# Performance work log

Hardware: AMD Instinct MI355X
Metric: run time of the kernel (lower is better)

The kernel has to match this reference:

```python
import jax, jax.numpy as jnp
import numpy as np

EPS = 1e-06
N_HEADS = 8


def setup_inputs() -> dict:
    key = jax.random.key(0)
    ks = jax.random.split(key, 9)
    B, M, T, C = 2, 64, 256, 512
    s = 0.02
    return {
        "x": jax.random.normal(ks[0], (B, M, T, C), dtype=jnp.float32),
        "Wq": jax.random.normal(ks[1], (C, C), dtype=jnp.float32) * s,
        "bq": jnp.zeros((C,), dtype=jnp.float32),
        "Wk": jax.random.normal(ks[2], (C, C), dtype=jnp.float32) * s,
        "bk": jnp.zeros((C,), dtype=jnp.float32),
        "Wv": jax.random.normal(ks[3], (C, C), dtype=jnp.float32) * s,
        "bv": jnp.zeros((C,), dtype=jnp.float32),
        "Wp": jax.random.normal(ks[4], (C, C), dtype=jnp.float32) * s,
        "bp": jnp.zeros((C,), dtype=jnp.float32),
    }


def _proj_heads(x, W, b, N, D):
    # nn.Linear: x @ W.T + b, then view(B,M,T,N,D).transpose(2,3) -> [B,M,N,T,D]
    B, M, T, C = x.shape
    y = jnp.einsum('bmtc,dc->bmtd', x, W) + b
    return y.reshape(B, M, T, N, D).transpose(0, 1, 3, 2, 4)


def reference(x, Wq, bq, Wk, bk, Wv, bv, Wp, bp):
    B, M, T, C = x.shape
    N = N_HEADS
    D = C // N
    q = _proj_heads(x, Wq, bq, N, D)  # [B,M,N,T,D]
    k = _proj_heads(x, Wk, bk, N, D)
    v = _proj_heads(x, Wv, bv, N, D)
    # ELU+1 feature map
    q = jax.nn.elu(q) + 1.0
    k = jax.nn.elu(k) + 1.0
    # KtV = k^T @ v : [B,M,N,D,D]
    KtV = jnp.einsum('bmntd,bmnte->bmnde', k, v)
    # Z = 1 / (q @ sum_t k + eps) : [B,M,N,T]
    ksum = jnp.sum(k, axis=-2)  # [B,M,N,D]
    z = 1.0 / (jnp.einsum('bmntd,bmnd->bmnt', q, ksum) + EPS)
    # Original does Z.expand(...,D) @ KtV; since Z is constant over the D axis,
    # this equals z[t] * sum_d KtV[d, e] -- compute that directly (faithful math).
    KtV_colsum = jnp.sum(KtV, axis=-2)  # [B,M,N,D]
    V = z[..., None] * KtV_colsum[..., None, :]  # [B,M,N,T,D]
    V = V.transpose(0, 1, 3, 2, 4).reshape(B, M, T, N * D)
    out = jnp.einsum('bmtc,dc->bmtd', V, Wp) + bp
    return out
```

## Files before the change

### kernel.cpp

```cpp
#include <hip/hip_runtime.h>
#include <hip/hip_bf16.h>

#define BM_ 128
#define T_  256
#define C_  512
#define NH  8
#define DH  64

typedef __bf16 bf16;
typedef __attribute__((ext_vector_type(8))) __bf16 bf16x8;
typedef __attribute__((ext_vector_type(4))) float f32x4;

__device__ __forceinline__ float elu1(float v){ return v > 0.f ? v + 1.f : __expf(v); }

__device__ __forceinline__ unsigned short f2bf(float f){
  unsigned u = __float_as_uint(f);
  u += 0x7fffu + ((u >> 16) & 1u);
  return (unsigned short)(u >> 16);
}

__device__ __forceinline__ float bf2f(unsigned short b){
  return __uint_as_float(((unsigned)b) << 16);
}

#define GLOAD16(gptr, lptr) __builtin_amdgcn_global_load_lds( \
  (const __attribute__((address_space(1))) void*)(gptr), \
  (__attribute__((address_space(3))) void*)(lptr), 16, 0, 0)

#define FENCE() asm volatile("" ::: "memory")

__global__ __launch_bounds__(256) void cvt3_kernel(
    const float* __restrict__ a, int na4,
    const float* __restrict__ b, int nb4,
    const float* __restrict__ c, int nc4,
    unsigned short* __restrict__ oa, unsigned short* __restrict__ ob,
    unsigned short* __restrict__ oc)
{
  int i = blockIdx.x * blockDim.x + threadIdx.x;
  int stride = gridDim.x * blockDim.x;
  int total = na4 + nb4 + nc4;
  for (; i < total; i += stride) {
    const float* src; unsigned short* dst; int idx;
    if (i < na4)            { src = a; dst = oa; idx = i; }
    else if (i < na4 + nb4) { src = b; dst = ob; idx = i - na4; }
    else                    { src = c; dst = oc; idx = i - na4 - nb4; }
    float4 v = reinterpret_cast<const float4*>(src)[idx];
    ushort4 o;
    o.x = f2bf(v.x); o.y = f2bf(v.y); o.z = f2bf(v.z); o.w = f2bf(v.w);
    reinterpret_cast<ushort4*>(dst)[idx] = o;
  }
}

template<int MODE>
__global__ __launch_bounds__(512, 2) void gemm_proj(
    const bf16* __restrict__ A, const bf16* __restrict__ Bw,
    const float* __restrict__ bias,
    float* __restrict__ krow, float* __restrict__ ksum2,
    const float* __restrict__ ksum2_in, float* __restrict__ zden)
{
  __shared__ bf16 As[2][256 * 64];
  __shared__ bf16 Bs[2][256 * 64];

  const int tid  = threadIdx.x;
  const int lane = tid & 63;
  const int wid  = tid >> 6;
  const int wr   = wid >> 2, wc = wid & 3;

  const int L  = ((blockIdx.x & 7) << 5) + (blockIdx.x >> 3);
  const int tn = L & 1, tm = L >> 1;

  const bf16* Ab = A  + (size_t)(tm * 256) * C_;
  const bf16* Bb = Bw + (size_t)(tn * 256) * C_;

  const int srow  = tid >> 3;
  const int sslot = tid & 7;
  const int fr = lane & 15, fq = lane >> 4;

  f32x4 acc[8][4];
#pragma unroll
  for (int m = 0; m < 8; ++m)
#pragma unroll
    for (int n = 0; n < 4; ++n) acc[m][n] = (f32x4){0.f, 0.f, 0.f, 0.f};

#define STG(XS, Xb, b, h, kt) do { \
  _Pragma("unroll") \
  for (int q = 0; q < 2; ++q) { \
    int r_ = (h) * 128 + q * 64 + srow; \
    GLOAD16(Xb + (size_t)r_ * C_ + (kt) * 64 + ((sslot ^ (r_ & 7)) << 3), \
            &XS[b][(((h) * 128 + q * 64) << 6) + (tid << 3)]); \
  } } while (0)

#define LOFF(row, sl) (((row) << 6) + ((((sl) ^ ((row) & 7))) << 3))

  STG(As, Ab, 0, 0, 0); STG(As, Ab, 0, 1, 0);
  STG(Bs, Bb, 0, 0, 0); STG(Bs, Bb, 0, 1, 0);
  asm volatile("s_waitcnt vmcnt(0)" ::: "memory");
  __builtin_amdgcn_s_barrier();
  FENCE();

  bf16x8 af[4][2], bfr[4][2];

  for (int t = 0; t < 8; ++t) {
    const int cur = t & 1;
    const bool pre = (t < 7);
#pragma unroll
    for (int m = 0; m < 4; ++m)
#pragma unroll
      for (int kk = 0; kk < 2; ++kk) {
        int row = wr * 128 + m * 16 + fr;
        af[m][kk] = *reinterpret_cast<const bf16x8*>(&As[cur][LOFF(row, kk * 4 + fq)]);
      }
#pragma unroll
    for (int n = 0; n < 2; ++n)
#pragma unroll
      for (int kk = 0; kk < 2; ++kk) {
        int row = wc * 64 + n * 16 + fr;
        bfr[n][kk] = *reinterpret_cast<const bf16x8*>(&Bs[cur][LOFF(row, kk * 4 + fq)]);
      }
    if (pre) { STG(As, Ab, cur ^ 1, 0, t + 1); STG(Bs, Bb, cur ^ 1, 0, t + 1); }
    __builtin_amdgcn_s_setprio(1);
#pragma unroll
    for (int m = 0; m < 4; ++m)
#pragma unroll
      for (int n = 0; n < 2; ++n)
#pragma unroll
        for (int kk = 0; kk < 2; ++kk)
          acc[m][n] = __builtin_amdgcn_mfma_f32_16x16x32_bf16(af[m][kk], bfr[n][kk], acc[m][n], 0, 0, 0);
    __builtin_amdgcn_s_setprio(0);
    __builtin_amdgcn_s_barrier();
    FENCE();
#pragma unroll
    for (int n = 0; n < 2; ++n)
#pragma unroll
      for (int kk = 0; kk < 2; ++kk) {
        int row = wc * 64 + (n + 2) * 16 + fr;
        bfr[n + 2][kk] = *reinterpret_cast<const bf16x8*>(&Bs[cur][LOFF(row, kk * 4 + fq)]);
      }
    if (pre) STG(As, Ab, cur ^ 1, 1, t + 1);
    __builtin_amdgcn_s_setprio(1);
#pragma unroll
    for (int m = 0; m < 4; ++m)
#pragma unroll
      for (int n = 0; n < 2; ++n)
#pragma unroll
        for (int kk = 0; kk < 2; ++kk)
          acc[m][n + 2] = __builtin_amdgcn_mfma_f32_16x16x32_bf16(af[m][kk], bfr[n + 2][kk], acc[m][n + 2], 0, 0, 0);
    __builtin_amdgcn_s_setprio(0);
    __builtin_amdgcn_s_barrier();
    FENCE();
#pragma unroll
    for (int m = 0; m < 4; ++m)
#pragma unroll
      for (int kk = 0; kk < 2; ++kk) {
        int row = wr * 128 + 64 + m * 16 + fr;
        af[m][kk] = *reinterpret_cast<const bf16x8*>(&As[cur][LOFF(row, kk * 4 + fq)]);
      }
    if (pre) STG(Bs, Bb, cur ^ 1, 1, t + 1);
    __builtin_amdgcn_s_setprio(1);
#pragma unroll
    for (int m = 0; m < 4; ++m)
#pragma unroll
      for (int n = 0; n < 2; ++n)
#pragma unroll
        for (int kk = 0; kk < 2; ++kk)
          acc[m + 4][n] = __builtin_amdgcn_mfma_f32_16x16x32_bf16(af[m][kk], bfr[n][kk], acc[m + 4][n], 0, 0, 0);
    __builtin_amdgcn_s_setprio(0);
    __builtin_amdgcn_s_barrier();
    FENCE();
    __builtin_amdgcn_s_setprio(1);
#pragma unroll
    for (int m = 0; m < 4; ++m)
#pragma unroll
      for (int n = 0; n < 2; ++n)
#pragma unroll
        for (int kk = 0; kk < 2; ++kk)
          acc[m + 4][n + 2] = __builtin_amdgcn_mfma_f32_16x16x32_bf16(af[m][kk], bfr[n + 2][kk], acc[m + 4][n + 2], 0, 0, 0);
    __builtin_amdgcn_s_setprio(0);
    asm volatile("s_waitcnt vmcnt(0)" ::: "memory");
    __builtin_amdgcn_s_barrier();
    FENCE();
  }
#undef STG
#undef LOFF

  const int bm   = tm;
  const int head = tn * 4 + wc;
  float bj[4];
#pragma unroll
  for (int n = 0; n < 4; ++n) bj[n] = bias[tn * 256 + wc * 64 + n * 16 + fr];

  if (MODE == 0) {
    float cs[4] = {0.f, 0.f, 0.f, 0.f};
#pragma unroll
    for (int m = 0; m < 8; ++m) {
#pragma unroll
      for (int r = 0; r < 4; ++r) {
        float rs = 0.f;
#pragma unroll
        for (int n = 0; n < 4; ++n) {
          float v = elu1(acc[m][n][r] + bj[n]);
          rs += v;
          cs[n] += v;
        }
#pragma unroll
        for (int msk = 1; msk < 16; msk <<= 1) rs += __shfl_xor(rs, msk);
        if (fr == 0) {
          int tg = wr * 128 + m * 16 + fq * 4 + r;
          krow[((size_t)bm * NH + head) * T_ + tg] = rs;
        }
      }
    }
#pragma unroll
    for (int n = 0; n < 4; ++n) {
      cs[n] += __shfl_xor(cs[n], 16);
      cs[n] += __shfl_xor(cs[n], 32);
      if (fq == 0)
        ksum2[((size_t)wr * BM_ + bm) * C_ + tn * 256 + wc * 64 + n * 16 + fr] = cs[n];
    }
  } else {
    float ks[4];
#pragma unroll
    for (int n = 0; n < 4; ++n) {
      size_t col = (size_t)bm * C_ + tn * 256 + wc * 64 + n * 16 + fr;
      ks[n] = ksum2_in[col] + ksum2_in[(size_t)BM_ * C_ + col];
    }
#pragma unroll
    for (int m = 0; m < 8; ++m) {
#pragma unroll
      for (int r = 0; r < 4; ++r) {
        float zs = 0.f;
#pragma unroll
        for (int n = 0; n < 4; ++n) zs = fmaf(elu1(acc[m][n][r] + bj[n]), ks[n], zs);
#pragma unroll
        for (int msk = 1; msk < 16; msk <<= 1) zs += __shfl_xor(zs, msk);
        if (fr == 0) {
          int tg = wr * 128 + m * 16 + fq * 4 + r;
          zden[((size_t)bm * NH + head) * T_ + tg] = zs;
        }
      }
    }
  }
}

__global__ __launch_bounds__(256) void xk_kernel(
    const unsigned short* __restrict__ xb, const float* __restrict__ krow,
    float* __restrict__ xk4, float* __restrict__ srow4)
{
  const int bm = blockIdx.x, qt = blockIdx.y, tid = threadIdx.x;
  __shared__ float krs[NH * 64];
#pragma unroll
  for (int p = 0; p < 2; ++p) {
    int idx = tid + p * 256;
    int n = idx >> 6, t = idx & 63;
    krs[idx] = krow[((size_t)bm * NH + n) * T_ + qt * 64 + t];
  }
  __syncthreads();
  float a0[8], a1[8];
#pragma unroll
  for (int n = 0; n < 8; ++n) { a0[n] = 0.f; a1[n] = 0.f; }
  const unsigned short* xp = xb + ((size_t)bm * T_ + qt * 64) * C_ + tid * 2;
  for (int t = 0; t < 64; ++t) {
    ushort2 u = *reinterpret_cast<const ushort2*>(xp + (size_t)t * C_);
    float x0 = bf2f(u.x), x1 = bf2f(u.y);
#pragma unroll
    for (int n = 0; n < 8; ++n) {
      float kr = krs[n * 64 + t];
      a0[n] = fmaf(kr, x0, a0[n]);
      a1[n] = fmaf(kr, x1, a1[n]);
    }
  }
#pragma unroll
  for (int n = 0; n < 8; ++n)
    *reinterpret_cast<float2*>(&xk4[(((size_t)qt * BM_ + bm) * NH + n) * C_ + tid * 2])
        = make_float2(a0[n], a1[n]);
  if (tid < 8) {
    float s = 0.f;
    for (int t = 0; t < 64; ++t) s += krs[tid * 64 + t];
    srow4[((size_t)qt * BM_ + bm) * NH + tid] = s;
  }
}

__global__ __launch_bounds__(256) void colsum_kernel(
    const float* __restrict__ xk4, const float* __restrict__ srow4,
    const float* __restrict__ Wv, const float* __restrict__ bv,
    float* __restrict__ cs_g)
{
  const int bm0 = blockIdx.x * 8, h = blockIdx.y, tid = threadIdx.x;
  __shared__ float4 xs4[8][128];
#pragma unroll
  for (int p = 0; p < 4; ++p) {
    int idx = tid + p * 256;
    int bmr = idx >> 7, c4 = idx & 127;
    float4 s = make_float4(0.f, 0.f, 0.f, 0.f);
#pragma unroll
    for (int q = 0; q < 4; ++q) {
      float4 u = *reinterpret_cast<const float4*>(
          xk4 + (((size_t)q * BM_ + bm0 + bmr) * NH + h) * C_ + c4 * 4);
      s.x += u.x; s.y += u.y; s.z += u.z; s.w += u.w;
    }
    xs4[bmr][c4] = s;
  }
  __syncthreads();
  const int e = tid & 63, bs = tid >> 6;
  const float4* wv4 = reinterpret_cast<const float4*>(Wv + (size_t)(h * DH + e) * C_);
  float acc0 = 0.f, acc1 = 0.f;
#pragma unroll 4
  for (int c4 = 0; c4 < 128; ++c4) {
    float4 w = wv4[c4];
    float4 a = xs4[bs * 2][c4];
    float4 b = xs4[bs * 2 + 1][c4];
    acc0 += w.x * a.x + w.y * a.y + w.z * a.z + w.w * a.w;
    acc1 += w.x * b.x + w.y * b.y + w.z * b.z + w.w * b.w;
  }
  float bve = bv[h * DH + e];
  int bmA = bm0 + bs * 2, bmB = bmA + 1;
  float sA = 0.f, sB = 0.f;
#pragma unroll
  for (int q = 0; q < 4; ++q) {
    sA += srow4[((size_t)q * BM_ + bmA) * NH + h];
    sB += srow4[((size_t)q * BM_ + bmB) * NH + h];
  }
  cs_g[((size_t)bmA * NH + h) * DH + e] = acc0 + sA * bve;
  cs_g[((size_t)bmB * NH + h) * DH + e] = acc1 + sB * bve;
}

__global__ __launch_bounds__(256) void wbuf_kernel(
    const float* __restrict__ cs_g, const float* __restrict__ Wp,
    float* __restrict__ wbuf)
{
  const int cpt = blockIdx.x, h = blockIdx.y, bm0 = blockIdx.z * 16;
  const int tid = threadIdx.x;
  __shared__ float4 csL4[16][16];
  {
    int bmr = tid >> 4, e4 = tid & 15;
    csL4[bmr][e4] = *reinterpret_cast<const float4*>(
        cs_g + ((size_t)(bm0 + bmr) * NH + h) * DH + e4 * 4);
  }
  __syncthreads();
  const int cp = cpt * 256 + tid;
  float4 wp[16];
  const float4* wpr = reinterpret_cast<const float4*>(Wp + (size_t)cp * C_ + h * DH);
#pragma unroll
  for (int e4 = 0; e4 < 16; ++e4) wp[e4] = wpr[e4];
#pragma unroll
  for (int bmr = 0; bmr < 16; ++bmr) {
    float acc = 0.f;
#pragma unroll
    for (int e4 = 0; e4 < 16; ++e4) {
      float4 c = csL4[bmr][e4];
      acc += wp[e4].x * c.x + wp[e4].y * c.y + wp[e4].z * c.z + wp[e4].w * c.w;
    }
    wbuf[((size_t)(bm0 + bmr) * NH + h) * C_ + cp] = acc;
  }
}

__global__ __launch_bounds__(256) void out_kernel(
    const float* __restrict__ zden, const float* __restrict__ wbuf,
    const float* __restrict__ bp, float* __restrict__ out)
{
  const int bm = blockIdx.x, tt = blockIdx.y, tid = threadIdx.x;
  __shared__ float zs[NH][64];
#pragma unroll
  for (int p = 0; p < 2; ++p) {
    int idx = tid + p * 256;
    int n = idx >> 6, t = idx & 63;
    zs[n][t] = 1.f / (zden[((size_t)bm * NH + n) * T_ + tt * 64 + t] + 1e-6f);
  }
  float2 wv[8];
  const int c2 = tid * 2;
#pragma unroll
  for (int n = 0; n < 8; ++n)
    wv[n] = *reinterpret_cast<const float2*>(wbuf + ((size_t)bm * NH + n) * C_ + c2);
  float2 bpv = *reinterpret_cast<const float2*>(bp + c2);
  __syncthreads();
  float* ob = out + ((size_t)bm * T_ + tt * 64) * C_;
  for (int t = 0; t < 64; ++t) {
    float o0 = bpv.x, o1 = bpv.y;
#pragma unroll
    for (int n = 0; n < 8; ++n) { float z = zs[n][t]; o0 = fmaf(z, wv[n].x, o0); o1 = fmaf(z, wv[n].y, o1); }
    *reinterpret_cast<float2*>(ob + (size_t)t * C_ + c2) = make_float2(o0, o1);
  }
}

extern "C" void kernel_launch(void* const* d_in, const int* in_sizes, int n_in,
                              void* d_out, int out_size, void* d_ws, size_t ws_size,
                              hipStream_t stream)
{
  const float* x  = (const float*)d_in[0];
  const float* Wq = (const float*)d_in[1];
  const float* bq = (const float*)d_in[2];
  const float* Wk = (const float*)d_in[3];
  const float* bk = (const float*)d_in[4];
  const float* Wv = (const float*)d_in[5];
  const float* bv = (const float*)d_in[6];
  const float* Wp = (const float*)d_in[7];
  const float* bp = (const float*)d_in[8];
  float* out = (float*)d_out;

  float* ws    = (float*)d_ws;
  float* zden  = ws;
  float* ksum2 = zden + 262144;
  float* krow  = ksum2 + 131072;
  float* srow4 = krow + 262144;
  float* xk4   = srow4 + 4096;
  float* cs    = xk4 + 2097152;
  float* wbuf  = cs + 65536;
  unsigned short* xb  = (unsigned short*)(wbuf + 524288);
  unsigned short* wkb = xb + 16777216;
  unsigned short* wqb = wkb + 262144;

  cvt3_kernel<<<2048, 256, 0, stream>>>(x, 16777216 / 4, Wk, 262144 / 4, Wq, 262144 / 4,
                                        xb, wkb, wqb);

  gemm_proj<0><<<256, 512, 0, stream>>>((const bf16*)xb, (const bf16*)wkb, bk,
                                        krow, ksum2, nullptr, nullptr);
  xk_kernel<<<dim3(BM_, 4), 256, 0, stream>>>(xb, krow, xk4, srow4);
  colsum_kernel<<<dim3(16, 8), 256, 0, stream>>>(xk4, srow4, Wv, bv, cs);
  wbuf_kernel<<<dim3(2, 8, 8), 256, 0, stream>>>(cs, Wp, wbuf);
  gemm_proj<1><<<256, 512, 0, stream>>>((const bf16*)xb, (const bf16*)wqb, bq,
                                        nullptr, nullptr, ksum2, zden);
  out_kernel<<<dim3(BM_, 4), 256, 0, stream>>>(zden, wbuf, bp, out);
}
```

Before: 115.9 us.

## Fuse K and Q projection GEMMs into one kernel sharing ksum through LDS

Merges the two separate projection GEMM launches (K with ELU row/column sums, Q with the z-denominator) into a single kernel. Each block runs the K main loop, reduces its column sums into shared memory, then reruns the main loop with the Q weights over the same x tile and computes zden from the on-chip ksum. This removes one kernel launch and the global ksum2 round trip. The main loop also drops the intermediate barriers between MFMA groups, leaving one per k-step, which cuts sync overhead but changes wave scheduling. The x tile is still reloaded from global (likely L2) for the second pass.

```diff
diff --git a/kernel.cpp b/kernel.cpp
--- a/kernel.cpp
+++ b/kernel.cpp
@@ -51,12 +51,11 @@
   }
 }
 
-template<int MODE>
-__global__ __launch_bounds__(512, 2) void gemm_proj(
-    const bf16* __restrict__ A, const bf16* __restrict__ Bw,
-    const float* __restrict__ bias,
-    float* __restrict__ krow, float* __restrict__ ksum2,
-    const float* __restrict__ ksum2_in, float* __restrict__ zden)
+__global__ __launch_bounds__(512, 2) void gemm_kq(
+    const bf16* __restrict__ A,
+    const bf16* __restrict__ Bk, const bf16* __restrict__ Bq,
+    const float* __restrict__ bk, const float* __restrict__ bq,
+    float* __restrict__ krow, float* __restrict__ zden)
 {
   __shared__ bf16 As[2][256 * 64];
   __shared__ bf16 Bs[2][256 * 64];
@@ -69,18 +68,15 @@
   const int L  = ((blockIdx.x & 7) << 5) + (blockIdx.x >> 3);
   const int tn = L & 1, tm = L >> 1;
 
-  const bf16* Ab = A  + (size_t)(tm * 256) * C_;
-  const bf16* Bb = Bw + (size_t)(tn * 256) * C_;
+  const bf16* Ab  = A  + (size_t)(tm * 256) * C_;
+  const bf16* Bkb = Bk + (size_t)(tn * 256) * C_;
+  const bf16* Bqb = Bq + (size_t)(tn * 256) * C_;
 
   const int srow  = tid >> 3;
   const int sslot = tid & 7;
   const int fr = lane & 15, fq = lane >> 4;
 
   f32x4 acc[8][4];
-#pragma unroll
-  for (int m = 0; m < 8; ++m)
-#pragma unroll
-    for (int n = 0; n < 4; ++n) acc[m][n] = (f32x4){0.f, 0.f, 0.f, 0.f};
 
 #define STG(XS, Xb, b, h, kt) do { \
   _Pragma("unroll") \
@@ -92,104 +88,109 @@
 
 #define LOFF(row, sl) (((row) << 6) + ((((sl) ^ ((row) & 7))) << 3))
 
+  bf16x8 af[4][2], bfr[4][2];
+
+  auto zero_acc = [&]() {
+#pragma unroll
+    for (int m = 0; m < 8; ++m)
+#pragma unroll
+      for (int n = 0; n < 4; ++n) acc[m][n] = (f32x4){0.f, 0.f, 0.f, 0.f};
+  };
+
+  auto main_loop = [&](const bf16* __restrict__ Bb) {
+    for (int t = 0; t < 8; ++t) {
+      const int cur = t & 1;
+      const bool pre = (t < 7);
+#pragma unroll
+      for (int m = 0; m < 4; ++m)
+#pragma unroll
+        for (int kk = 0; kk < 2; ++kk) {
+          int row = wr * 128 + m * 16 + fr;
+          af[m][kk] = *reinterpret_cast<const bf16x8*>(&As[cur][LOFF(row, kk * 4 + fq)]);
+        }
+#pragma unroll
+      for (int n = 0; n < 2; ++n)
+#pragma unroll
+        for (int kk = 0; kk < 2; ++kk) {
+          int row = wc * 64 + n * 16 + fr;
+          bfr[n][kk] = *reinterpret_cast<const bf16x8*>(&Bs[cur][LOFF(row, kk * 4 + fq)]);
+        }
+      if (pre) { STG(As, Ab, cur ^ 1, 0, t + 1); STG(Bs, Bb, cur ^ 1, 0, t + 1); }
+      __builtin_amdgcn_s_setprio(1);
+#pragma unroll
+      for (int m = 0; m < 4; ++m)
+#pragma unroll
+        for (int n = 0; n < 2; ++n)
+#pragma unroll
+          for (int kk = 0; kk < 2; ++kk)
+            acc[m][n] = __builtin_amdgcn_mfma_f32_16x16x32_bf16(af[m][kk], bfr[n][kk], acc[m][n], 0, 0, 0);
+      __builtin_amdgcn_s_setprio(0);
+#pragma unroll
+      for (int n = 0; n < 2; ++n)
+#pragma unroll
+        for (int kk = 0; kk < 2; ++kk) {
+          int row = wc * 64 + (n + 2) * 16 + fr;
+          bfr[n + 2][kk] = *reinterpret_cast<const bf16x8*>(&Bs[cur][LOFF(row, kk * 4 + fq)]);
+        }
+      if (pre) STG(As, Ab, cur ^ 1, 1, t + 1);
+      __builtin_amdgcn_s_setprio(1);
+#pragma unroll
+      for (int m = 0; m < 4; ++m)
+#pragma unroll
+        for (int n = 0; n < 2; ++n)
+#pragma unroll
+          for (int kk = 0; kk < 2; ++kk)
+            acc[m][n + 2] = __builtin_amdgcn_mfma_f32_16x16x32_bf16(af[m][kk], bfr[n + 2][kk], acc[m][n + 2], 0, 0, 0);
+      __builtin_amdgcn_s_setprio(0);
+#pragma unroll
+      for (int m = 0; m < 4; ++m)
+#pragma unroll
+        for (int kk = 0; kk < 2; ++kk) {
+          int row = wr * 128 + 64 + m * 16 + fr;
+          af[m][kk] = *reinterpret_cast<const bf16x8*>(&As[cur][LOFF(row, kk * 4 + fq)]);
+        }
+      if (pre) STG(Bs, Bb, cur ^ 1, 1, t + 1);
+      __builtin_amdgcn_s_setprio(1);
+#pragma unroll
+      for (int m = 0; m < 4; ++m)
+#pragma unroll
+        for (int n = 0; n < 2; ++n)
+#pragma unroll
+          for (int kk = 0; kk < 2; ++kk)
+            acc[m + 4][n] = __builtin_amdgcn_mfma_f32_16x16x32_bf16(af[m][kk], bfr[n][kk], acc[m + 4][n], 0, 0, 0);
+      __builtin_amdgcn_s_setprio(0);
+      __builtin_amdgcn_s_setprio(1);
+#pragma unroll
+      for (int m = 0; m < 4; ++m)
+#pragma unroll
+        for (int n = 0; n < 2; ++n)
+#pragma unroll
+          for (int kk = 0; kk < 2; ++kk)
+            acc[m + 4][n + 2] = __builtin_amdgcn_mfma_f32_16x16x32_bf16(af[m][kk], bfr[n + 2][kk], acc[m + 4][n + 2], 0, 0, 0);
+      __builtin_amdgcn_s_setprio(0);
+      asm volatile("s_waitcnt vmcnt(0)" ::: "memory");
+      __builtin_amdgcn_s_barrier();
+      FENCE();
+    }
+  };
+
+  zero_acc();
   STG(As, Ab, 0, 0, 0); STG(As, Ab, 0, 1, 0);
-  STG(Bs, Bb, 0, 0, 0); STG(Bs, Bb, 0, 1, 0);
+  STG(Bs, Bkb, 0, 0, 0); STG(Bs, Bkb, 0, 1, 0);
   asm volatile("s_waitcnt vmcnt(0)" ::: "memory");
   __builtin_amdgcn_s_barrier();
   FENCE();
-
-  bf16x8 af[4][2], bfr[4][2];
-
-  for (int t = 0; t < 8; ++t) {
-    const int cur = t & 1;
-    const bool pre = (t < 7);
-#pragma unroll
-    for (int m = 0; m < 4; ++m)
-#pragma unroll
-      for (int kk = 0; kk < 2; ++kk) {
-        int row = wr * 128 + m * 16 + fr;
-        af[m][kk] = *reinterpret_cast<const bf16x8*>(&As[cur][LOFF(row, kk * 4 + fq)]);
-      }
-#pragma unroll
-    for (int n = 0; n < 2; ++n)
-#pragma unroll
-      for (int kk = 0; kk < 2; ++kk) {
-        int row = wc * 64 + n * 16 + fr;
-        bfr[n][kk] = *reinterpret_cast<const bf16x8*>(&Bs[cur][LOFF(row, kk * 4 + fq)]);
-      }
-    if (pre) { STG(As, Ab, cur ^ 1, 0, t + 1); STG(Bs, Bb, cur ^ 1, 0, t + 1); }
-    __builtin_amdgcn_s_setprio(1);
-#pragma unroll
-    for (int m = 0; m < 4; ++m)
-#pragma unroll
-      for (int n = 0; n < 2; ++n)
-#pragma unroll
-        for (int kk = 0; kk < 2; ++kk)
-          acc[m][n] = __builtin_amdgcn_mfma_f32_16x16x32_bf16(af[m][kk], bfr[n][kk], acc[m][n], 0, 0, 0);
-    __builtin_amdgcn_s_setprio(0);
-    __builtin_amdgcn_s_barrier();
-    FENCE();
-#pragma unroll
-    for (int n = 0; n < 2; ++n)
-#pragma unroll
-      for (int kk = 0; kk < 2; ++kk) {
-        int row = wc * 64 + (n + 2) * 16 + fr;
-        bfr[n + 2][kk] = *reinterpret_cast<const bf16x8*>(&Bs[cur][LOFF(row, kk * 4 + fq)]);
-      }
-    if (pre) STG(As, Ab, cur ^ 1, 1, t + 1);
-    __builtin_amdgcn_s_setprio(1);
-#pragma unroll
-    for (int m = 0; m < 4; ++m)
-#pragma unroll
-      for (int n = 0; n < 2; ++n)
-#pragma unroll
-        for (int kk = 0; kk < 2; ++kk)
-          acc[m][n + 2] = __builtin_amdgcn_mfma_f32_16x16x32_bf16(af[m][kk], bfr[n + 2][kk], acc[m][n + 2], 0, 0, 0);
-    __builtin_amdgcn_s_setprio(0);
-    __builtin_amdgcn_s_barrier();
-    FENCE();
-#pragma unroll
-    for (int m = 0; m < 4; ++m)
-#pragma unroll
-      for (int kk = 0; kk < 2; ++kk) {
-        int row = wr * 128 + 64 + m * 16 + fr;
-        af[m][kk] = *reinterpret_cast<const bf16x8*>(&As[cur][LOFF(row, kk * 4 + fq)]);
-      }
-    if (pre) STG(Bs, Bb, cur ^ 1, 1, t + 1);
-    __builtin_amdgcn_s_setprio(1);
-#pragma unroll
-    for (int m = 0; m < 4; ++m)
-#pragma unroll
-      for (int n = 0; n < 2; ++n)
-#pragma unroll
-        for (int kk = 0; kk < 2; ++kk)
-          acc[m + 4][n] = __builtin_amdgcn_mfma_f32_16x16x32_bf16(af[m][kk], bfr[n][kk], acc[m + 4][n], 0, 0, 0);
-    __builtin_amdgcn_s_setprio(0);
-    __builtin_amdgcn_s_barrier();
-    FENCE();
-    __builtin_amdgcn_s_setprio(1);
-#pragma unroll
-    for (int m = 0; m < 4; ++m)
-#pragma unroll
-      for (int n = 0; n < 2; ++n)
-#pragma unroll
-        for (int kk = 0; kk < 2; ++kk)
-          acc[m + 4][n + 2] = __builtin_amdgcn_mfma_f32_16x16x32_bf16(af[m][kk], bfr[n + 2][kk], acc[m + 4][n + 2], 0, 0, 0);
-    __builtin_amdgcn_s_setprio(0);
-    asm volatile("s_waitcnt vmcnt(0)" ::: "memory");
-    __builtin_amdgcn_s_barrier();
-    FENCE();
-  }
-#undef STG
-#undef LOFF
+  main_loop(Bkb);
+
+  STG(As, Ab, 0, 0, 0); STG(As, Ab, 0, 1, 0);
 
   const int bm   = tm;
   const int head = tn * 4 + wc;
-  float bj[4];
-#pragma unroll
-  for (int n = 0; n < 4; ++n) bj[n] = bias[tn * 256 + wc * 64 + n * 16 + fr];
-
-  if (MODE == 0) {
+  float* ksum_sh = reinterpret_cast<float*>(&Bs[0][0]);
+  {
+    float bj[4];
+#pragma unroll
+    for (int n = 0; n < 4; ++n) bj[n] = bk[tn * 256 + wc * 64 + n * 16 + fr];
     float cs[4] = {0.f, 0.f, 0.f, 0.f};
 #pragma unroll
     for (int m = 0; m < 8; ++m) {
@@ -215,15 +216,34 @@
       cs[n] += __shfl_xor(cs[n], 16);
       cs[n] += __shfl_xor(cs[n], 32);
       if (fq == 0)
-        ksum2[((size_t)wr * BM_ + bm) * C_ + tn * 256 + wc * 64 + n * 16 + fr] = cs[n];
-    }
-  } else {
-    float ks[4];
-#pragma unroll
-    for (int n = 0; n < 4; ++n) {
-      size_t col = (size_t)bm * C_ + tn * 256 + wc * 64 + n * 16 + fr;
-      ks[n] = ksum2_in[col] + ksum2_in[(size_t)BM_ * C_ + col];
-    }
+        ksum_sh[wr * 256 + wc * 64 + n * 16 + fr] = cs[n];
+    }
+  }
+  asm volatile("s_waitcnt lgkmcnt(0)" ::: "memory");
+  __builtin_amdgcn_s_barrier();
+  FENCE();
+
+  float ks[4];
+#pragma unroll
+  for (int n = 0; n < 4; ++n) {
+    int col = wc * 64 + n * 16 + fr;
+    ks[n] = ksum_sh[col] + ksum_sh[256 + col];
+  }
+  asm volatile("s_waitcnt lgkmcnt(0)" ::: "memory");
+  __builtin_amdgcn_s_barrier();
+  FENCE();
+
+  zero_acc();
+  STG(Bs, Bqb, 0, 0, 0); STG(Bs, Bqb, 0, 1, 0);
+  asm volatile("s_waitcnt vmcnt(0)" ::: "memory");
+  __builtin_amdgcn_s_barrier();
+  FENCE();
+  main_loop(Bqb);
+
+  {
+    float bj[4];
+#pragma unroll
+    for (int n = 0; n < 4; ++n) bj[n] = bq[tn * 256 + wc * 64 + n * 16 + fr];
 #pragma unroll
     for (int m = 0; m < 8; ++m) {
 #pragma unroll
@@ -240,6 +260,8 @@
       }
     }
   }
+#undef STG
+#undef LOFF
 }
 
 __global__ __launch_bounds__(256) void xk_kernel(
@@ -399,8 +421,7 @@
 
   float* ws    = (float*)d_ws;
   float* zden  = ws;
-  float* ksum2 = zden + 262144;
-  float* krow  = ksum2 + 131072;
+  float* krow  = zden + 262144;
   float* srow4 = krow + 262144;
   float* xk4   = srow4 + 4096;
   float* cs    = xk4 + 2097152;
@@ -412,12 +433,10 @@
   cvt3_kernel<<<2048, 256, 0, stream>>>(x, 16777216 / 4, Wk, 262144 / 4, Wq, 262144 / 4,
                                         xb, wkb, wqb);
 
-  gemm_proj<0><<<256, 512, 0, stream>>>((const bf16*)xb, (const bf16*)wkb, bk,
-                                        krow, ksum2, nullptr, nullptr);
+  gemm_kq<<<256, 512, 0, stream>>>((const bf16*)xb, (const bf16*)wkb, (const bf16*)wqb,
+                                   bk, bq, krow, zden);
   xk_kernel<<<dim3(BM_, 4), 256, 0, stream>>>(xb, krow, xk4, srow4);
   colsum_kernel<<<dim3(16, 8), 256, 0, stream>>>(xk4, srow4, Wv, bv, cs);
   wbuf_kernel<<<dim3(2, 8, 8), 256, 0, stream>>>(cs, Wp, wbuf);
-  gemm_proj<1><<<256, 512, 0, stream>>>((const bf16*)xb, (const bf16*)wqb, bq,
-                                        nullptr, nullptr, ksum2, zden);
   out_kernel<<<dim3(BM_, 4), 256, 0, stream>>>(zden, wbuf, bp, out);
 }
```

After: 130.3 us. 12.4% more time.
